# Kernel tuning notes

Hardware: AMD Instinct MI355X
Metric: run time of the kernel (lower is better)

## Reference

```python
import jax, jax.numpy as jnp
import numpy as np


def _flip_roll(a):
    # torch.roll(torch.flip(a, [-3,-2,-1]), (1,1,1), [-3,-2,-1])
    return jnp.roll(jnp.flip(a, axis=(-3, -2, -1)), shift=(1, 1, 1), axis=(-3, -2, -1))


def dht_3d(x):
    dims = (2, 3, 4)
    r = jnp.fft.fftn(x, axes=dims).real - jnp.fft.fftn(jnp.flip(x, axis=-1), axes=dims).imag
    norm = jnp.sqrt(jnp.sum(r * r, axis=dims, keepdims=True))
    safe = jnp.where(norm == 0, 1.0, norm)
    return jnp.where(norm != 0, r / safe, jnp.zeros_like(r))


def compl_mul3d(x1, x2):
    x1n = _flip_roll(x1)
    x2n = _flip_roll(x2)
    return 0.5 * (
        jnp.einsum('bixyz,ioxyz->boxyz', x1, x2)
        - jnp.einsum('bixyz,ioxyz->boxyz', x1n, x2n)
        + jnp.einsum('bixyz,ioxyz->boxyz', x1, x2n)
        + jnp.einsum('bixyz,ioxyz->boxyz', x1n, x2)
    )


def idht_3d(X):
    n = X.shape[2] * X.shape[3] * X.shape[4]
    return dht_3d(X) / n


def setup_inputs() -> dict:
    key = jax.random.key(0)
    k1, k2 = jax.random.split(key)
    B, Cin, Cout = 4, 32, 32
    S = 64
    M = 8
    scale = 1.0 / (Cin * Cout)
    x = jax.random.normal(k1, (B, Cin, S, S, S), dtype=jnp.float32)
    weights1 = scale * jax.random.uniform(k2, (Cin, Cout, M, M, M), dtype=jnp.float32)
    return {"x": x, "weights1": weights1}


def reference(x, weights1):
    B = x.shape[0]
    Cout = weights1.shape[1]
    m1, m2, m3 = weights1.shape[2], weights1.shape[3], weights1.shape[4]
    s1, s2, s3 = x.shape[-3], x.shape[-2], x.shape[-1]
    x_ht = dht_3d(x)
    conv = compl_mul3d(x_ht[:, :, :m1, :m2, :m3], weights1)
    out_ht = jnp.zeros((B, Cout, s1, s2, s3), dtype=x.dtype)
    out_ht = out_ht.at[:, :, :m1, :m2, :m3].set(conv)
    return idht_3d(out_ht)
```

## Files before the change

kernel.cpp:

```cpp
#include <hip/hip_runtime.h>
#include <math.h>


constexpr int NT = 262144;
constexpr float TWOPI_64 = 0.09817477042468103f;


__global__ __launch_bounds__(256) void k_fwd1(const float* __restrict__ x,
                                              float* __restrict__ S,
                                              float* __restrict__ red1p) {
  __shared__ float As[64 * 68];
  __shared__ float Bs[64 * 68];
  __shared__ float PL[32 * 65];
  __shared__ float c64v[64], s64v[64];
  __shared__ float rsm[12];
  const int t = threadIdx.x;
  const int j = blockIdx.x;
  const int bc = blockIdx.y;
  const int n1a = j, n1b = (64 - j) & 63;
  const bool paired = (n1a != n1b);
  if (t < 64) { float ang = TWOPI_64 * t; c64v[t] = cosf(ang); s64v[t] = sinf(ang); }
  const float4* xa4 = (const float4*)(x + ((size_t)bc << 18) + (n1a << 12));
  const float4* xb4 = (const float4*)(x + ((size_t)bc << 18) + (n1b << 12));
  float ssp = 0.f;
  for (int q = 0; q < 4; ++q) {
    int l4 = t + (q << 8);
    int fl = l4 << 2;
    int r = fl >> 6, c = fl & 63;
    float4 va = xa4[l4], vb = xb4[l4];
    *(float4*)&As[r * 68 + c] = va;
    *(float4*)&Bs[r * 68 + c] = vb;
    ssp += va.x * va.x + va.y * va.y + va.z * va.z + va.w * va.w;
    if (paired) ssp += vb.x * vb.x + vb.y * vb.y + vb.z * vb.z + vb.w * vb.w;
  }
  __syncthreads();
  const int n2 = t & 63;
  const int k3a = t >> 6, k3b = k3a + 4;
  {
    float ca = 1.f, sa = 0.f, cb = 1.f, sb = 0.f;
    const float dca = c64v[k3a], dsa = s64v[k3a];
    const float dcb = c64v[k3b], dsb = s64v[k3b];
    float reA0 = 0, imA0 = 0, reA1 = 0, imA1 = 0;
    float reB0 = 0, imB0 = 0, reB1 = 0, imB1 = 0;
    const float4* Ar = (const float4*)&As[n2 * 68];
    const float4* Br = (const float4*)&Bs[n2 * 68];
    for (int m = 0; m < 16; ++m) {
      float4 va = Ar[m], vb = Br[m];
      float av[4] = {va.x, va.y, va.z, va.w};
      float bv[4] = {vb.x, vb.y, vb.z, vb.w};
#pragma unroll
      for (int e = 0; e < 4; ++e) {
        float a = av[e], b = bv[e];
        reA0 += a * ca; imA0 -= a * sa;
        reB0 += b * ca; imB0 -= b * sa;
        reA1 += a * cb; imA1 -= a * sb;
        reB1 += b * cb; imB1 -= b * sb;
        float nca = ca * dca - sa * dsa; sa = sa * dca + ca * dsa; ca = nca;
        float ncb = cb * dcb - sb * dsb; sb = sb * dcb + cb * dsb; cb = ncb;
      }
    }
    PL[(k3a) * 65 + n2] = reA0;      PL[(8 + k3a) * 65 + n2] = imA0;
    PL[(16 + k3a) * 65 + n2] = reB0; PL[(24 + k3a) * 65 + n2] = imB0;
    PL[(k3b) * 65 + n2] = reA1;      PL[(8 + k3b) * 65 + n2] = imA1;
    PL[(16 + k3b) * 65 + n2] = reB1; PL[(24 + k3b) * 65 + n2] = imB1;
  }
  float c1p = 0.f, c2p = 0.f;
  for (int q = 0; q < 16; ++q) {
    int l = t + (q << 8);
    int r = l >> 6, c = l & 63;
    float a = As[r * 68 + c];
    int m2 = (64 - r) & 63;
    int m3 = (64 - c) & 63;
    int m3b = (62 - c) & 63;
    c1p += a * Bs[m2 * 68 + m3];
    c2p += a * Bs[m2 * 68 + m3b];
  }
  if (paired) { c1p *= 2.f; c2p *= 2.f; }
  for (int off = 32; off; off >>= 1) {
    ssp += __shfl_down(ssp, off);
    c1p += __shfl_down(c1p, off);
    c2p += __shfl_down(c2p, off);
  }
  const int lane = t & 63, wid = t >> 6;
  if (lane == 0) { rsm[wid * 3] = ssp; rsm[wid * 3 + 1] = c1p; rsm[wid * 3 + 2] = c2p; }
  __syncthreads();
  if (t == 0) {
    red1p[((size_t)bc * 33 + j) * 3 + 0] = rsm[0] + rsm[3] + rsm[6] + rsm[9];
    red1p[((size_t)bc * 33 + j) * 3 + 1] = rsm[1] + rsm[4] + rsm[7] + rsm[10];
    red1p[((size_t)bc * 33 + j) * 3 + 2] = rsm[2] + rsm[5] + rsm[8] + rsm[11];
  }
  {
    const int k2 = t & 7;
    const int rr = t >> 3;
    const int row = rr >> 4, f = (rr >> 3) & 1, k3 = rr & 7;
    float rc = 1.f, rs = 0.f;
    const float dc = c64v[k2], ds = s64v[k2];
    float re = 0.f, im = 0.f;
    const float* pr = &PL[rr * 65];
    for (int n2i = 0; n2i < 64; ++n2i) {
      float v = pr[n2i];
      re += v * rc; im -= v * rs;
      float nc = rc * dc - rs * ds; rs = rs * dc + rc * ds; rc = nc;
    }
    const int n1row = row ? n1b : n1a;
    ((float2*)S)[(((size_t)bc * 64 + n1row) * 2 + f) * 64 + k2 * 8 + k3] =
        make_float2(re, im);
  }
}

__global__ __launch_bounds__(256) void k_fwd2s(const float* __restrict__ S,
                                               const float* __restrict__ red1p,
                                               float* __restrict__ xh) {
  __shared__ float2 U3L[512];
  __shared__ float c64v[64], s64v[64];
  __shared__ float rbuf[99];
  const int t = threadIdx.x;
  const int h = blockIdx.x;
  const int bc = blockIdx.y;
  if (t < 64) { float ang = TWOPI_64 * t; c64v[t] = cosf(ang); s64v[t] = sinf(ang); }
  if (t < 99) rbuf[t] = red1p[(size_t)bc * 99 + t];
  __syncthreads();
  {
    const int kkl = t & 31;
    const int f = (t >> 5) & 1;
    const int k1g = t >> 6;
    const int rr2 = f * 64 + h * 32 + kkl;
    const float2* Sb = (const float2*)(S + ((size_t)bc << 14));
    float rc[2], rs[2], dc[2], ds[2], re[2], im[2];
#pragma unroll
    for (int m = 0; m < 2; ++m) {
      int k1 = k1g * 2 + m;
      rc[m] = 1.f; rs[m] = 0.f; dc[m] = c64v[k1]; ds[m] = s64v[k1];
      re[m] = 0.f; im[m] = 0.f;
    }
#pragma unroll 4
    for (int n1 = 0; n1 < 64; ++n1) {
      float2 ab = Sb[(n1 << 7) + rr2];
#pragma unroll
      for (int m = 0; m < 2; ++m) {
        re[m] += ab.x * rc[m] + ab.y * rs[m];
        im[m] += ab.y * rc[m] - ab.x * rs[m];
        float nc = rc[m] * dc[m] - rs[m] * ds[m];
        rs[m] = rs[m] * dc[m] + rc[m] * ds[m];
        rc[m] = nc;
      }
    }
#pragma unroll
    for (int m = 0; m < 2; ++m) {
      int k1 = k1g * 2 + m;
      U3L[f * 256 + k1 * 32 + kkl] = make_float2(re[m], im[m]);
    }
  }
  __syncthreads();
  float ss = 0.f, c1 = 0.f, c2 = 0.f;
  for (int jj = 0; jj < 33; ++jj) {
    ss += rbuf[jj * 3];
    c1 += rbuf[jj * 3 + 1];
    c2 += rbuf[jj * 3 + 2];
  }
  float nsq = 0.5f * (float)NT * (2.f * ss + c1 - c2);
  float inv1 = nsq > 0.f ? rsqrtf(nsq) : 0.f;
  {
    const int k1 = t >> 5, kkl = t & 31;
    const int kk = h * 32 + kkl;
    const int k3 = kk & 7;
    float2 U = U3L[k1 * 32 + kkl];
    float2 V = U3L[256 + k1 * 32 + kkl];
    float ct = c64v[k3], st = s64v[k3];
    float r = U.x - V.y - st * (U.x + V.y) - ct * (U.y - V.x);
    xh[(size_t)bc * 512 + k1 * 64 + kk] = r * inv1;
  }
}

__global__ __launch_bounds__(256) void k_mixA(const float* __restrict__ xh,
                                              const float* __restrict__ w,
                                              float* __restrict__ A1,
                                              float* __restrict__ inv2) {
  __shared__ float xsh[16384];
  const int t = threadIdx.x;
  const int bc2 = blockIdx.x;
  const int b = bc2 >> 5, o = bc2 & 31;
  const float4* xb4 = (const float4*)(xh + ((size_t)b << 14));
  float4* xs4 = (float4*)xsh;
  for (int q = 0; q < 16; ++q) xs4[t + (q << 8)] = xb4[t + (q << 8)];
  __syncthreads();
  float acc0 = 0.f, acc1 = 0.f;
  {
    int k0 = t, kq1 = t + 256;
    int k1 = k0 >> 6, k2 = (k0 >> 3) & 7, k3 = k0 & 7;
    int nk0 = (((8 - k1) & 7) << 6) + (((8 - k2) & 7) << 3) + ((8 - k3) & 7);
    int l1 = kq1 >> 6, l2 = (kq1 >> 3) & 7, l3 = kq1 & 7;
    int nk1 = (((8 - l1) & 7) << 6) + (((8 - l2) & 7) << 3) + ((8 - l3) & 7);
    for (int i = 0; i < 32; ++i) {
      const float* wr = w + (((size_t)i * 32 + o) << 9);
      float xa0 = xsh[(i << 9) + k0],  xn0 = xsh[(i << 9) + nk0];
      float xa1 = xsh[(i << 9) + kq1], xn1 = xsh[(i << 9) + nk1];
      acc0 += (xa0 + xn0) * wr[k0]  + (xa0 - xn0) * wr[nk0];
      acc1 += (xa1 + xn1) * wr[kq1] + (xa1 - xn1) * wr[nk1];
    }
  }
  __syncthreads();
  xsh[t] = 0.5f * acc0;
  xsh[t + 256] = 0.5f * acc1;
  if (t < 64) {
    float ang = TWOPI_64 * t;
    xsh[512 + t] = cosf(ang);
    xsh[576 + t] = sinf(ang);
  }
  __syncthreads();
  const int col = t & 63;
  const int quarter = t >> 6;
  float cv[8];
#pragma unroll
  for (int n1 = 0; n1 < 8; ++n1) cv[n1] = xsh[(n1 << 6) + col];
  if (quarter == 0) {
    float p = 0.f;
#pragma unroll
    for (int n1 = 0; n1 < 8; ++n1) p += cv[n1] * cv[n1];
    for (int off = 32; off; off >>= 1) p += __shfl_down(p, off);
    if (t == 0) {
      float c000 = cv[0];
      float nsq = 0.5f * (float)NT * (2.f * p + c000 * c000);
      float nrm = sqrtf(nsq);
      inv2[bc2] = nrm > 0.f ? 1.f / (nrm * (float)NT) : 0.f;
    }
  }
  float2* A1p = (float2*)(A1 + ((size_t)bc2 << 13));
  for (int it = 0; it < 16; ++it) {
    int k1 = quarter + (it << 2);
    float re = 0.f, im = 0.f;
#pragma unroll
    for (int n1 = 0; n1 < 8; ++n1) {
      int a = (k1 * n1) & 63;
      re += cv[n1] * xsh[512 + a];
      im -= cv[n1] * xsh[576 + a];
    }
    A1p[(k1 << 6) + col] = make_float2(re, im);
  }
}

__global__ __launch_bounds__(256) void k_expBC(const float* __restrict__ A1,
                                               const float* __restrict__ inv2,
                                               float* __restrict__ out) {
  __shared__ float arow[128];
  __shared__ float B2[64 * 20];
  __shared__ float c64v[64], s64v[64];
  const int t = threadIdx.x;
  const int k1 = blockIdx.x;
  const int bc2 = blockIdx.y;
  if (t < 64) { float ang = TWOPI_64 * t; c64v[t] = cosf(ang); s64v[t] = sinf(ang); }
  if (t < 128) arow[t] = A1[((size_t)bc2 << 13) + (k1 << 7) + t];
  __syncthreads();
  {
    const int k2 = t & 63;
    const int g = t >> 6;
    const int f = g & 1;
    const int n3h = (g >> 1) << 2;
    float acc[4] = {0, 0, 0, 0};
    for (int n2i = 0; n2i < 8; ++n2i) {
      int a_ = (k2 * n2i) & 63;
      float tc = c64v[a_], ts = s64v[a_];
      const float4* ar4 = (const float4*)&arow[((n2i << 3) + n3h) << 1];
      float4 p0 = ar4[0];
      float4 p1 = ar4[1];
      if (f == 0) {
        acc[0] += p0.x * tc + p0.y * ts;
        acc[1] += p0.z * tc + p0.w * ts;
        acc[2] += p1.x * tc + p1.y * ts;
        acc[3] += p1.z * tc + p1.w * ts;
      } else {
        acc[0] += p0.y * tc - p0.x * ts;
        acc[1] += p0.w * tc - p0.z * ts;
        acc[2] += p1.y * tc - p1.x * ts;
        acc[3] += p1.w * tc - p1.z * ts;
      }
    }
    *(float4*)&B2[k2 * 20 + (f << 3) + n3h] = make_float4(acc[0], acc[1], acc[2], acc[3]);
  }
  __syncthreads();
  {
    const int k3 = t & 63;
    const int wid = t >> 6;
    float C1r[8], C2r[8];
#pragma unroll
    for (int n3 = 0; n3 < 8; ++n3) {
      int a0 = (k3 * n3) & 63;
      int a1 = (k3 * (n3 + 1)) & 63;
      C1r[n3] = c64v[a0] - s64v[a1];
      C2r[n3] = s64v[a0] - c64v[a1];
    }
    const float sc = inv2[bc2];
    float* dst = out + ((size_t)bc2 << 18) + (k1 << 12);
    for (int it = 0; it < 16; ++it) {
      int k2 = (wid << 4) + it;
      const float4* br4 = (const float4*)&B2[k2 * 20];
      float4 r0 = br4[0], r1 = br4[1], r2 = br4[2], r3 = br4[3];
      float acc = r0.x * C1r[0] + r0.y * C1r[1] + r0.z * C1r[2] + r0.w * C1r[3]
                + r1.x * C1r[4] + r1.y * C1r[5] + r1.z * C1r[6] + r1.w * C1r[7]
                + r2.x * C2r[0] + r2.y * C2r[1] + r2.z * C2r[2] + r2.w * C2r[3]
                + r3.x * C2r[4] + r3.y * C2r[5] + r3.z * C2r[6] + r3.w * C2r[7];
      dst[(k2 << 6) + k3] = acc * sc;
    }
  }
}

extern "C" void kernel_launch(void* const* d_in, const int* in_sizes, int n_in,
                              void* d_out, int out_size, void* d_ws, size_t ws_size,
                              hipStream_t stream) {
  const float* x = (const float*)d_in[0];
  const float* w = (const float*)d_in[1];
  float* out = (float*)d_out;
  float* ws = (float*)d_ws;
  float* S     = ws;
  float* red1p = ws + 2097152;
  float* xh    = ws + 2109824;
  float* inv2  = ws + 2175360;
  float* A1    = ws + 2175488;

  k_fwd1 <<<dim3(33, 128), 256, 0, stream>>>(x, S, red1p);
  k_fwd2s<<<dim3(2, 128),  256, 0, stream>>>(S, red1p, xh);
  k_mixA <<<dim3(128),     256, 0, stream>>>(xh, w, A1, inv2);
  k_expBC<<<dim3(64, 128), 256, 0, stream>>>(A1, inv2, out);
}
```

Before: 274.5 us.

## Use even/odd symmetric folding and twiddle table lookups in first-stage DFT

The first forward kernel's partial DFTs along the last two axes now pre-fold each row into symmetric sums and differences (x[m]+x[64-m], x[m]-x[64-m]). That halves the multiply-accumulate count, and twiddle factors come from a shared cos/sin table instead of being advanced by rotation in registers. Raw input is stored in a single padded shared array (stride 71), and the folding for the two halves of n2 is staged through a shared buffer. This adds extra syncthreads phases and scalar shared-memory stores in place of float4 stores.

```diff
diff --git a/kernel.cpp b/kernel.cpp
--- a/kernel.cpp
+++ b/kernel.cpp
@@ -9,17 +9,20 @@
 __global__ __launch_bounds__(256) void k_fwd1(const float* __restrict__ x,
                                               float* __restrict__ S,
                                               float* __restrict__ red1p) {
-  __shared__ float As[64 * 68];
-  __shared__ float Bs[64 * 68];
+  __shared__ float Raw[128 * 71];
+  __shared__ float4 F1h[33 * 32];
   __shared__ float PL[32 * 65];
-  __shared__ float c64v[64], s64v[64];
+  __shared__ float2 ct64[64];
   __shared__ float rsm[12];
+  float2* F2 = (float2*)F1h;
+
   const int t = threadIdx.x;
   const int j = blockIdx.x;
   const int bc = blockIdx.y;
   const int n1a = j, n1b = (64 - j) & 63;
   const bool paired = (n1a != n1b);
-  if (t < 64) { float ang = TWOPI_64 * t; c64v[t] = cosf(ang); s64v[t] = sinf(ang); }
+  if (t < 64) { float ang = TWOPI_64 * t; ct64[t] = make_float2(cosf(ang), sinf(ang)); }
+
   const float4* xa4 = (const float4*)(x + ((size_t)bc << 18) + (n1a << 12));
   const float4* xb4 = (const float4*)(x + ((size_t)bc << 18) + (n1b << 12));
   float ssp = 0.f;
@@ -28,52 +31,41 @@
     int fl = l4 << 2;
     int r = fl >> 6, c = fl & 63;
     float4 va = xa4[l4], vb = xb4[l4];
-    *(float4*)&As[r * 68 + c] = va;
-    *(float4*)&Bs[r * 68 + c] = vb;
+    Raw[r * 71 + c] = va.x; Raw[r * 71 + c + 1] = va.y;
+    Raw[r * 71 + c + 2] = va.z; Raw[r * 71 + c + 3] = va.w;
+    Raw[(64 + r) * 71 + c] = vb.x; Raw[(64 + r) * 71 + c + 1] = vb.y;
+    Raw[(64 + r) * 71 + c + 2] = vb.z; Raw[(64 + r) * 71 + c + 3] = vb.w;
     ssp += va.x * va.x + va.y * va.y + va.z * va.z + va.w * va.w;
     if (paired) ssp += vb.x * vb.x + vb.y * vb.y + vb.z * vb.z + vb.w * vb.w;
   }
   __syncthreads();
-  const int n2 = t & 63;
-  const int k3a = t >> 6, k3b = k3a + 4;
-  {
-    float ca = 1.f, sa = 0.f, cb = 1.f, sb = 0.f;
-    const float dca = c64v[k3a], dsa = s64v[k3a];
-    const float dcb = c64v[k3b], dsb = s64v[k3b];
-    float reA0 = 0, imA0 = 0, reA1 = 0, imA1 = 0;
-    float reB0 = 0, imB0 = 0, reB1 = 0, imB1 = 0;
-    const float4* Ar = (const float4*)&As[n2 * 68];
-    const float4* Br = (const float4*)&Bs[n2 * 68];
-    for (int m = 0; m < 16; ++m) {
-      float4 va = Ar[m], vb = Br[m];
-      float av[4] = {va.x, va.y, va.z, va.w};
-      float bv[4] = {vb.x, vb.y, vb.z, vb.w};
-#pragma unroll
-      for (int e = 0; e < 4; ++e) {
-        float a = av[e], b = bv[e];
-        reA0 += a * ca; imA0 -= a * sa;
-        reB0 += b * ca; imB0 -= b * sa;
-        reA1 += a * cb; imA1 -= a * sb;
-        reB1 += b * cb; imB1 -= b * sb;
-        float nca = ca * dca - sa * dsa; sa = sa * dca + ca * dsa; ca = nca;
-        float ncb = cb * dcb - sb * dsb; sb = sb * dcb + cb * dsb; cb = ncb;
-      }
-    }
-    PL[(k3a) * 65 + n2] = reA0;      PL[(8 + k3a) * 65 + n2] = imA0;
-    PL[(16 + k3a) * 65 + n2] = reB0; PL[(24 + k3a) * 65 + n2] = imB0;
-    PL[(k3b) * 65 + n2] = reA1;      PL[(8 + k3b) * 65 + n2] = imA1;
-    PL[(16 + k3b) * 65 + n2] = reB1; PL[(24 + k3b) * 65 + n2] = imB1;
+
+  {
+    const int n2p = t & 31, g = t >> 5;
+    const int n2 = n2p;
+#pragma unroll
+    for (int e = 0; e < 4; ++e) {
+      int m = g * 4 + e;
+      if (m == 0) {
+        F1h[n2p] = make_float4(Raw[n2 * 71], Raw[n2 * 71 + 32],
+                               Raw[(64 + n2) * 71], Raw[(64 + n2) * 71 + 32]);
+      } else {
+        float a1 = Raw[n2 * 71 + m], a2 = Raw[n2 * 71 + 64 - m];
+        float b1 = Raw[(64 + n2) * 71 + m], b2 = Raw[(64 + n2) * 71 + 64 - m];
+        F1h[m * 32 + n2p] = make_float4(a1 + a2, a1 - a2, b1 + b2, b1 - b2);
+      }
+    }
   }
   float c1p = 0.f, c2p = 0.f;
   for (int q = 0; q < 16; ++q) {
     int l = t + (q << 8);
     int r = l >> 6, c = l & 63;
-    float a = As[r * 68 + c];
+    float a = Raw[r * 71 + c];
     int m2 = (64 - r) & 63;
     int m3 = (64 - c) & 63;
     int m3b = (62 - c) & 63;
-    c1p += a * Bs[m2 * 68 + m3];
-    c2p += a * Bs[m2 * 68 + m3b];
+    c1p += a * Raw[(64 + m2) * 71 + m3];
+    c2p += a * Raw[(64 + m2) * 71 + m3b];
   }
   if (paired) { c1p *= 2.f; c2p *= 2.f; }
   for (int off = 32; off; off >>= 1) {
@@ -81,27 +73,91 @@
     c1p += __shfl_down(c1p, off);
     c2p += __shfl_down(c2p, off);
   }
-  const int lane = t & 63, wid = t >> 6;
-  if (lane == 0) { rsm[wid * 3] = ssp; rsm[wid * 3 + 1] = c1p; rsm[wid * 3 + 2] = c2p; }
-  __syncthreads();
-  if (t == 0) {
-    red1p[((size_t)bc * 33 + j) * 3 + 0] = rsm[0] + rsm[3] + rsm[6] + rsm[9];
-    red1p[((size_t)bc * 33 + j) * 3 + 1] = rsm[1] + rsm[4] + rsm[7] + rsm[10];
-    red1p[((size_t)bc * 33 + j) * 3 + 2] = rsm[2] + rsm[5] + rsm[8] + rsm[11];
-  }
-  {
-    const int k2 = t & 7;
-    const int rr = t >> 3;
+  {
+    const int lane = t & 63, wid = t >> 6;
+    if (lane == 0) { rsm[wid * 3] = ssp; rsm[wid * 3 + 1] = c1p; rsm[wid * 3 + 2] = c2p; }
+  }
+  __syncthreads();
+
+#pragma unroll
+  for (int h = 0; h < 2; ++h) {
+    {
+      const int n2p = t & 31, k3 = t >> 5;
+      const int n2 = h * 32 + n2p;
+      const float sg = (k3 & 1) ? -1.f : 1.f;
+      float4 f0 = F1h[n2p];
+      float reA = f0.x + sg * f0.y, imA = 0.f;
+      float reB = f0.z + sg * f0.w, imB = 0.f;
+      int jj = k3;
+      for (int m = 1; m < 32; ++m) {
+        float4 f4 = F1h[m * 32 + n2p];
+        float2 tw = ct64[jj];
+        reA += f4.x * tw.x; imA -= f4.y * tw.y;
+        reB += f4.z * tw.x; imB -= f4.w * tw.y;
+        jj = (jj + k3) & 63;
+      }
+      PL[k3 * 65 + n2] = reA;
+      PL[(8 + k3) * 65 + n2] = imA;
+      PL[(16 + k3) * 65 + n2] = reB;
+      PL[(24 + k3) * 65 + n2] = imB;
+    }
+    if (h == 0) {
+      if (t == 0) {
+        red1p[((size_t)bc * 33 + j) * 3 + 0] = rsm[0] + rsm[3] + rsm[6] + rsm[9];
+        red1p[((size_t)bc * 33 + j) * 3 + 1] = rsm[1] + rsm[4] + rsm[7] + rsm[10];
+        red1p[((size_t)bc * 33 + j) * 3 + 2] = rsm[2] + rsm[5] + rsm[8] + rsm[11];
+      }
+      __syncthreads();
+      {
+        const int n2p = t & 31, g = t >> 5;
+        const int n2 = 32 + n2p;
+#pragma unroll
+        for (int e = 0; e < 4; ++e) {
+          int m = g * 4 + e;
+          if (m == 0) {
+            F1h[n2p] = make_float4(Raw[n2 * 71], Raw[n2 * 71 + 32],
+                                   Raw[(64 + n2) * 71], Raw[(64 + n2) * 71 + 32]);
+          } else {
+            float a1 = Raw[n2 * 71 + m], a2 = Raw[n2 * 71 + 64 - m];
+            float b1 = Raw[(64 + n2) * 71 + m], b2 = Raw[(64 + n2) * 71 + 64 - m];
+            F1h[m * 32 + n2p] = make_float4(a1 + a2, a1 - a2, b1 + b2, b1 - b2);
+          }
+        }
+      }
+      __syncthreads();
+    }
+  }
+  __syncthreads();
+
+  {
+    const int rr = t & 31, g = t >> 5;
+#pragma unroll
+    for (int e = 0; e < 4; ++e) {
+      int m = g * 4 + e;
+      if (m == 0) {
+        F2[rr] = make_float2(PL[rr * 65], PL[rr * 65 + 32]);
+      } else {
+        float p1 = PL[rr * 65 + m], p2 = PL[rr * 65 + 64 - m];
+        F2[m * 32 + rr] = make_float2(p1 + p2, p1 - p2);
+      }
+    }
+  }
+  __syncthreads();
+
+  {
+    const int rr = t & 31, k2 = t >> 5;
+    const float sg = (k2 & 1) ? -1.f : 1.f;
+    float2 e0 = F2[rr];
+    float re = e0.x + sg * e0.y, im = 0.f;
+    int jj = k2;
+    for (int m = 1; m < 32; ++m) {
+      float2 d = F2[m * 32 + rr];
+      float2 tw = ct64[jj];
+      re += d.x * tw.x;
+      im -= d.y * tw.y;
+      jj = (jj + k2) & 63;
+    }
     const int row = rr >> 4, f = (rr >> 3) & 1, k3 = rr & 7;
-    float rc = 1.f, rs = 0.f;
-    const float dc = c64v[k2], ds = s64v[k2];
-    float re = 0.f, im = 0.f;
-    const float* pr = &PL[rr * 65];
-    for (int n2i = 0; n2i < 64; ++n2i) {
-      float v = pr[n2i];
-      re += v * rc; im -= v * rs;
-      float nc = rc * dc - rs * ds; rs = rs * dc + rc * ds; rc = nc;
-    }
     const int n1row = row ? n1b : n1a;
     ((float2*)S)[(((size_t)bc * 64 + n1row) * 2 + f) * 64 + k2 * 8 + k3] =
         make_float2(re, im);
```

Result: no change. 276.3 us (+0.7%).
